# Kernel optimization log

Hardware: AMD Instinct MI355X
Metric: run time of the kernel (lower is better)

The kernel has to match this reference:

```python
import jax, jax.numpy as jnp
import numpy as np

S, K, O = 8192, 1024, 4096  # seq_len, in_features, out_features


def setup_inputs() -> dict:
    key = jax.random.key(0)
    k1, k2, k3, k4, k5 = jax.random.split(key, 5)
    x = jax.random.randint(k1, (S, K), -128, 128, dtype=jnp.int8)
    weight_q = jax.random.randint(k2, (O, K), -128, 128, dtype=jnp.int8)
    scale_x = jax.random.uniform(k3, (), jnp.float32, 0.01, 0.1)
    scale_w = jax.random.uniform(k4, (), jnp.float32, 0.01, 0.1)
    scale_y = jax.random.uniform(k5, (S,), jnp.float32, 0.5, 2.0)  # per-row output scale
    return {"x": x, "weight_q": weight_q, "scale_x": scale_x,
            "scale_w": scale_w, "scale_y": scale_y}


def reference(x, weight_q, scale_x, scale_w, scale_y):
    # int8 GEMM with int32 accumulation: [S,K] @ [O,K]^T -> [S,O]
    acc = jnp.einsum('sk,ok->so', x.astype(jnp.int32), weight_q.astype(jnp.int32))
    # fused per-row requantization: scale_y[:seq_len] gives per-row scale
    requant_scale = (scale_x * scale_w / scale_y).astype(jnp.float32)  # [S]
    scaled = acc.astype(jnp.float32) * requant_scale[:, None]
    out_q = jnp.clip(jnp.round(scaled), -128.0, 127.0).astype(jnp.int8)
    return out_q, scale_y
```

## Files before the change

kernel.cpp:

```cpp
#include <hip/hip_runtime.h>


#define S_DIM 8192
#define K_DIM 1024
#define O_DIM 4096
#define BM 128
#define BN 128
#define BK 64
#define NITER (K_DIM / BK)
#define TILE_BYTES (BM * BK)

using i32x4 = __attribute__((ext_vector_type(4))) int;

__device__ __forceinline__ void load_lds16(const void* g, void* l) {
  __builtin_amdgcn_global_load_lds(
      (const __attribute__((address_space(1))) void*)g,
      (__attribute__((address_space(3))) void*)l, 16, 0, 0);
}

__global__ void pack_kernel(const int* __restrict__ xi, const int* __restrict__ wi,
                            const float* __restrict__ sy,
                            uint4* __restrict__ ap, uint4* __restrict__ bp,
                            float* __restrict__ out_sy) {
  const int tid = blockIdx.x * blockDim.x + threadIdx.x;
  const int nA = S_DIM * K_DIM / 16;
  const int nB = O_DIM * K_DIM / 16;

  const int* src;
  uint4* dst;
  int j;
  if (tid < nA) {
    src = xi; dst = ap; j = tid;
  } else if (tid < nA + nB) {
    src = wi; dst = bp; j = tid - nA;
  } else {
    return;
  }
  const int t = j >> 9;
  const int idx = j & 511;
  const int r = idx >> 2;
  const int cs = idx & 3;
  const int c = cs ^ (r & 3);
  const int band = t >> 4;
  const int kt = t & 15;
  const int row = band * 128 + r;
  const int4* s4 = (const int4*)src + row * 256 + kt * 16 + c * 4;
  int4 v0 = s4[0], v1 = s4[1], v2 = s4[2], v3 = s4[3];
  uint4 o;
  o.x = (v0.x & 0xff) | ((v0.y & 0xff) << 8) | ((v0.z & 0xff) << 16) | (((unsigned)v0.w & 0xff) << 24);
  o.y = (v1.x & 0xff) | ((v1.y & 0xff) << 8) | ((v1.z & 0xff) << 16) | (((unsigned)v1.w & 0xff) << 24);
  o.z = (v2.x & 0xff) | ((v2.y & 0xff) << 8) | ((v2.z & 0xff) << 16) | (((unsigned)v2.w & 0xff) << 24);
  o.w = (v3.x & 0xff) | ((v3.y & 0xff) << 8) | ((v3.z & 0xff) << 16) | (((unsigned)v3.w & 0xff) << 24);
  dst[j] = o;
  if (tid < S_DIM) out_sy[tid] = sy[tid];
}

__global__ __launch_bounds__(256, 4) void gemm_i8_kernel(
    const signed char* __restrict__ Ap,
    const signed char* __restrict__ Bp,
    const float* __restrict__ sx, const float* __restrict__ sw,
    const float* __restrict__ sy, float* __restrict__ out) {
  __shared__ __align__(16) signed char As[2][TILE_BYTES];
  __shared__ __align__(16) signed char Bs[2][TILE_BYTES];

  const int tid = threadIdx.x;
  const int wave = tid >> 6;
  const int lane = tid & 63;
  const int wm = wave >> 1;
  const int wn = wave & 1;
  const int rowBase = blockIdx.x * BM;
  const int colBase = blockIdx.y * BN;

  const int soff = wave * 1024 + lane * 16;
  const signed char* gA = Ap + (size_t)blockIdx.x * NITER * TILE_BYTES + soff;
  const signed char* gB = Bp + (size_t)blockIdx.y * NITER * TILE_BYTES + soff;
  signed char* ldsA = (signed char*)As + wave * 1024;
  signed char* ldsB = (signed char*)Bs + wave * 1024;

  i32x4 acc[4][4] = {};

  const int fr = lane & 15;
  const int fq = (((lane >> 4) ^ (fr & 3)) & 3) * 16;

  load_lds16(gA, ldsA);
  load_lds16(gA + 4096, ldsA + 4096);
  load_lds16(gB, ldsB);
  load_lds16(gB + 4096, ldsB + 4096);

  for (int it = 0; it < NITER; ++it) {
    __syncthreads();

    if (it + 1 < NITER) {
      const int boff = ((it + 1) & 1) * TILE_BYTES;
      const size_t goff = (size_t)(it + 1) * TILE_BYTES;
      load_lds16(gA + goff, ldsA + boff);
      load_lds16(gA + goff + 4096, ldsA + boff + 4096);
      load_lds16(gB + goff, ldsB + boff);
      load_lds16(gB + goff + 4096, ldsB + boff + 4096);
    }

    const signed char* curA = As[it & 1];
    const signed char* curB = Bs[it & 1];
    i32x4 bf[4];
#pragma unroll
    for (int ni = 0; ni < 4; ++ni)
      bf[ni] = *(const i32x4*)(curB + (wn * 64 + ni * 16 + fr) * BK + fq);

#pragma unroll
    for (int mi = 0; mi < 4; ++mi) {
      i32x4 af = *(const i32x4*)(curA + (wm * 64 + mi * 16 + fr) * BK + fq);
#pragma unroll
      for (int ni = 0; ni < 4; ++ni)
        acc[mi][ni] =
            __builtin_amdgcn_mfma_i32_16x16x64_i8(af, bf[ni], acc[mi][ni], 0, 0, 0);
    }
  }

  const float sxw = sx[0] * sw[0];
  const int quad = lane >> 4;
#pragma unroll
  for (int mi = 0; mi < 4; ++mi) {
#pragma unroll
    for (int r = 0; r < 4; ++r) {
      const int s = rowBase + wm * 64 + mi * 16 + quad * 4 + r;
      const float rs = sxw / sy[s];
      float* orow = out + (size_t)s * O_DIM + colBase + wn * 64 + fr;
#pragma unroll
      for (int ni = 0; ni < 4; ++ni) {
        float f = rintf((float)acc[mi][ni][r] * rs);
        f = fminf(127.0f, fmaxf(-128.0f, f));
        orow[ni * 16] = f;
      }
    }
  }
}

extern "C" void kernel_launch(void* const* d_in, const int* in_sizes, int n_in,
                              void* d_out, int out_size, void* d_ws, size_t ws_size,
                              hipStream_t stream) {
  const int* x = (const int*)d_in[0];
  const int* w = (const int*)d_in[1];
  const float* sx = (const float*)d_in[2];
  const float* sw = (const float*)d_in[3];
  const float* sy = (const float*)d_in[4];
  float* out = (float*)d_out;

  uint4* ap = (uint4*)d_ws;
  uint4* bp = ap + (size_t)S_DIM * K_DIM / 16;

  const int total = S_DIM * K_DIM / 16 + O_DIM * K_DIM / 16;
  pack_kernel<<<(total + 255) / 256, 256, 0, stream>>>(
      x, w, sy, ap, bp, out + (size_t)S_DIM * O_DIM);

  dim3 grid(S_DIM / BM, O_DIM / BN);
  gemm_i8_kernel<<<grid, 256, 0, stream>>>(
      (const signed char*)ap, (const signed char*)bp, sx, sw, sy, out);
}
```

Baseline: 200.9 us.

## Load A fragments directly from global into registers, bypassing LDS

The pack kernel now lays out A in MFMA fragment order (sub-tile, quad, row) so each lane can read its A operand straight from global memory into registers. This removes the A tile from LDS, halving LDS traffic and the shared-memory footprint, and double-buffers the A fragments in registers. The cost is that each of the two wn waves reads the same A data from global/L2 separately, and register pressure goes up.

```diff
diff --git a/kernel.cpp b/kernel.cpp
--- a/kernel.cpp
+++ b/kernel.cpp
@@ -26,32 +26,35 @@
   const int nA = S_DIM * K_DIM / 16;
   const int nB = O_DIM * K_DIM / 16;
 
-  const int* src;
-  uint4* dst;
-  int j;
+  const int4* s4 = nullptr;
+  uint4* dst = nullptr;
+  int j = 0;
   if (tid < nA) {
-    src = xi; dst = ap; j = tid;
+    j = tid;
+    const int t = j >> 9, idx = j & 511;
+    const int sub = idx >> 6, q = (idx >> 4) & 3, fr = idx & 15;
+    const int band = t >> 4, kt = t & 15;
+    const int row = band * 128 + sub * 16 + fr;
+    s4 = (const int4*)xi + row * 256 + kt * 16 + q * 4;
+    dst = ap;
   } else if (tid < nA + nB) {
-    src = wi; dst = bp; j = tid - nA;
-  } else {
-    return;
+    j = tid - nA;
+    const int t = j >> 9, idx = j & 511;
+    const int r = idx >> 2, cs = idx & 3, c = cs ^ (r & 3);
+    const int band = t >> 4, kt = t & 15;
+    const int row = band * 128 + r;
+    s4 = (const int4*)wi + row * 256 + kt * 16 + c * 4;
+    dst = bp;
   }
-  const int t = j >> 9;
-  const int idx = j & 511;
-  const int r = idx >> 2;
-  const int cs = idx & 3;
-  const int c = cs ^ (r & 3);
-  const int band = t >> 4;
-  const int kt = t & 15;
-  const int row = band * 128 + r;
-  const int4* s4 = (const int4*)src + row * 256 + kt * 16 + c * 4;
-  int4 v0 = s4[0], v1 = s4[1], v2 = s4[2], v3 = s4[3];
-  uint4 o;
-  o.x = (v0.x & 0xff) | ((v0.y & 0xff) << 8) | ((v0.z & 0xff) << 16) | (((unsigned)v0.w & 0xff) << 24);
-  o.y = (v1.x & 0xff) | ((v1.y & 0xff) << 8) | ((v1.z & 0xff) << 16) | (((unsigned)v1.w & 0xff) << 24);
-  o.z = (v2.x & 0xff) | ((v2.y & 0xff) << 8) | ((v2.z & 0xff) << 16) | (((unsigned)v2.w & 0xff) << 24);
-  o.w = (v3.x & 0xff) | ((v3.y & 0xff) << 8) | ((v3.z & 0xff) << 16) | (((unsigned)v3.w & 0xff) << 24);
-  dst[j] = o;
+  if (s4) {
+    int4 v0 = s4[0], v1 = s4[1], v2 = s4[2], v3 = s4[3];
+    uint4 o;
+    o.x = (v0.x & 0xff) | ((v0.y & 0xff) << 8) | ((v0.z & 0xff) << 16) | (((unsigned)v0.w & 0xff) << 24);
+    o.y = (v1.x & 0xff) | ((v1.y & 0xff) << 8) | ((v1.z & 0xff) << 16) | (((unsigned)v1.w & 0xff) << 24);
+    o.z = (v2.x & 0xff) | ((v2.y & 0xff) << 8) | ((v2.z & 0xff) << 16) | (((unsigned)v2.w & 0xff) << 24);
+    o.w = (v3.x & 0xff) | ((v3.y & 0xff) << 8) | ((v3.z & 0xff) << 16) | (((unsigned)v3.w & 0xff) << 24);
+    dst[j] = o;
+  }
   if (tid < S_DIM) out_sy[tid] = sy[tid];
 }
 
@@ -60,7 +63,6 @@
     const signed char* __restrict__ Bp,
     const float* __restrict__ sx, const float* __restrict__ sw,
     const float* __restrict__ sy, float* __restrict__ out) {
-  __shared__ __align__(16) signed char As[2][TILE_BYTES];
   __shared__ __align__(16) signed char Bs[2][TILE_BYTES];
 
   const int tid = threadIdx.x;
@@ -72,47 +74,46 @@
   const int colBase = blockIdx.y * BN;
 
   const int soff = wave * 1024 + lane * 16;
-  const signed char* gA = Ap + (size_t)blockIdx.x * NITER * TILE_BYTES + soff;
   const signed char* gB = Bp + (size_t)blockIdx.y * NITER * TILE_BYTES + soff;
-  signed char* ldsA = (signed char*)As + wave * 1024;
   signed char* ldsB = (signed char*)Bs + wave * 1024;
+
+  const signed char* gA = Ap + (size_t)blockIdx.x * NITER * TILE_BYTES +
+                          wm * 4096 + lane * 16;
 
   i32x4 acc[4][4] = {};
 
   const int fr = lane & 15;
   const int fq = (((lane >> 4) ^ (fr & 3)) & 3) * 16;
 
-  load_lds16(gA, ldsA);
-  load_lds16(gA + 4096, ldsA + 4096);
   load_lds16(gB, ldsB);
   load_lds16(gB + 4096, ldsB + 4096);
+  i32x4 af[2][4];
+#pragma unroll
+  for (int mi = 0; mi < 4; ++mi)
+    af[0][mi] = *(const i32x4*)(gA + mi * 1024);
 
   for (int it = 0; it < NITER; ++it) {
+    const int p = it & 1;
     __syncthreads();
 
     if (it + 1 < NITER) {
       const int boff = ((it + 1) & 1) * TILE_BYTES;
       const size_t goff = (size_t)(it + 1) * TILE_BYTES;
-      load_lds16(gA + goff, ldsA + boff);
-      load_lds16(gA + goff + 4096, ldsA + boff + 4096);
       load_lds16(gB + goff, ldsB + boff);
       load_lds16(gB + goff + 4096, ldsB + boff + 4096);
+#pragma unroll
+      for (int mi = 0; mi < 4; ++mi)
+        af[p ^ 1][mi] = *(const i32x4*)(gA + goff + mi * 1024);
     }
 
-    const signed char* curA = As[it & 1];
     const signed char* curB = Bs[it & 1];
-    i32x4 bf[4];
 #pragma unroll
-    for (int ni = 0; ni < 4; ++ni)
-      bf[ni] = *(const i32x4*)(curB + (wn * 64 + ni * 16 + fr) * BK + fq);
-
+    for (int ni = 0; ni < 4; ++ni) {
+      i32x4 bf = *(const i32x4*)(curB + (wn * 64 + ni * 16 + fr) * BK + fq);
 #pragma unroll
-    for (int mi = 0; mi < 4; ++mi) {
-      i32x4 af = *(const i32x4*)(curA + (wm * 64 + mi * 16 + fr) * BK + fq);
-#pragma unroll
-      for (int ni = 0; ni < 4; ++ni)
+      for (int mi = 0; mi < 4; ++mi)
         acc[mi][ni] =
-            __builtin_amdgcn_mfma_i32_16x16x64_i8(af, bf[ni], acc[mi][ni], 0, 0, 0);
+            __builtin_amdgcn_mfma_i32_16x16x64_i8(af[p][mi], bf, acc[mi][ni], 0, 0, 0);
     }
   }
 
```

Result: no change. 201.1 us (+0.1%).
